# Kernel optimization log

Hardware: AMD Instinct MI355X
Metric: run time of the kernel (lower is better)

## Reference

```python
import jax, jax.numpy as jnp
import numpy as np

N_NODES = 100000
N_EDGES = 1600000
IN_DIM, HID_DIM, OUT_DIM = 128, 64, 64


def _graph_conv(src, dst, h, W, b, n_nodes):
    # DGL GraphConv, norm='both': out = D_in^{-1/2} A (D_out^{-1/2} h W) + b
    ones = jnp.ones(src.shape[0], dtype=h.dtype)
    deg_out = jax.ops.segment_sum(ones, src, num_segments=n_nodes)
    deg_in = jax.ops.segment_sum(ones, dst, num_segments=n_nodes)
    norm_src = jax.lax.rsqrt(jnp.maximum(deg_out, 1.0))  # [N]
    norm_dst = jax.lax.rsqrt(jnp.maximum(deg_in, 1.0))   # [N]
    # project first (in_dim >= out_dim path), then aggregate over edges
    x = (h * norm_src[:, None]) @ W                      # [N, d_out]
    msg = x[src]                                         # [E, d_out] gather
    agg = jax.ops.segment_sum(msg, dst, num_segments=n_nodes)  # [N, d_out]
    return agg * norm_dst[:, None] + b


def setup_inputs() -> dict:
    key = jax.random.key(0)
    k = jax.random.split(key, 6)
    h = jax.random.normal(k[0], (N_NODES, IN_DIM), dtype=jnp.float32)
    src = jax.random.randint(k[1], (N_EDGES,), 0, N_NODES, dtype=jnp.int32)
    dst = jax.random.randint(k[2], (N_EDGES,), 0, N_NODES, dtype=jnp.int32)
    W1 = jax.random.normal(k[3], (IN_DIM, HID_DIM), dtype=jnp.float32) / np.sqrt(IN_DIM)
    b1 = jnp.zeros((HID_DIM,), dtype=jnp.float32)
    W2 = jax.random.normal(k[4], (HID_DIM, OUT_DIM), dtype=jnp.float32) / np.sqrt(HID_DIM)
    b2 = jnp.zeros((OUT_DIM,), dtype=jnp.float32)
    return {"h": h, "src": src, "dst": dst, "W1": W1, "b1": b1, "W2": W2, "b2": b2}


def reference(h, src, dst, W1, b1, W2, b2):
    x = _graph_conv(src, dst, h, W1, b1, N_NODES)
    x = jax.nn.elu(x)  # act = nn.ELU()
    x = _graph_conv(src, dst, x, W2, b2, N_NODES)
    return x  # last_act is None
```

## Files before the change

kernel.cpp:

```cpp
#include <hip/hip_runtime.h>
#include <math.h>

#define CH 4096
#define NBUK_MAX 256
#define MAXB 12288
#define SRC_BITS 17

typedef short bf16x8 __attribute__((ext_vector_type(8)));
typedef float f32x4 __attribute__((ext_vector_type(4)));
typedef float f32x2 __attribute__((ext_vector_type(2)));

__device__ __forceinline__ unsigned short f2bf(float f) {
    union { float f; unsigned int u; } v; v.f = f;
    unsigned int r = (v.u + 0x7FFFu + ((v.u >> 16) & 1u)) >> 16;
    return (unsigned short)r;
}
__device__ __forceinline__ float bf2f(unsigned short u) {
    union { unsigned int u; float f; } v; v.u = ((unsigned int)u) << 16;
    return v.f;
}
__device__ __forceinline__ float bflo(unsigned int u) {
    union { unsigned int u; float f; } v; v.u = u << 16;
    return v.f;
}
__device__ __forceinline__ float bfhi(unsigned int u) {
    union { unsigned int u; float f; } v; v.u = u & 0xFFFF0000u;
    return v.f;
}

__global__ __launch_bounds__(256) void p1a_kernel(const int* __restrict__ src, const int* __restrict__ dst,
                                                  int* __restrict__ mat, int E, int B1, int nbuk) {
    __shared__ int hd[NBUK_MAX], hs[NBUK_MAX];
    const int t = threadIdx.x;
    if (t < nbuk) { hd[t] = 0; hs[t] = 0; }
    __syncthreads();
    const int base = blockIdx.x * CH;
    const int cnt = min(CH, E - base);
    for (int k = t; k < cnt; k += 256) {
        int d = dst[base + k];
        int s = src[base + k];
        atomicAdd(&hd[d >> 9], 1);
        atomicAdd(&hs[s >> 9], 1);
    }
    __syncthreads();
    if (t < nbuk) {
        mat[t * B1 + blockIdx.x] = hd[t];
        mat[(nbuk + t) * B1 + blockIdx.x] = hs[t];
    }
}

__global__ __launch_bounds__(256) void scan1_kernel(const int* __restrict__ cnt,
                                                    int* __restrict__ seg,
                                                    int* __restrict__ bsums, int N) {
    __shared__ int tsum[256];
    const int t = threadIdx.x;
    const int base = blockIdx.x * 1024 + t * 4;
    int v0 = (base + 0 < N) ? cnt[base + 0] : 0;
    int v1 = (base + 1 < N) ? cnt[base + 1] : 0;
    int v2 = (base + 2 < N) ? cnt[base + 2] : 0;
    int v3 = (base + 3 < N) ? cnt[base + 3] : 0;
    tsum[t] = v0 + v1 + v2 + v3;
    __syncthreads();
    for (int off = 1; off < 256; off <<= 1) {
        int x = (t >= off) ? tsum[t - off] : 0;
        __syncthreads();
        if (t >= off) tsum[t] += x;
        __syncthreads();
    }
    int run = (t > 0) ? tsum[t - 1] : 0;
    if (base + 0 < N) seg[base + 0] = run; run += v0;
    if (base + 1 < N) seg[base + 1] = run; run += v1;
    if (base + 2 < N) seg[base + 2] = run; run += v2;
    if (base + 3 < N) seg[base + 3] = run;
    if (t == 255) bsums[blockIdx.x] = tsum[255];
}

__global__ void scan2_kernel(int* __restrict__ bsums, int* __restrict__ seg, int N, int G) {
    __shared__ int s[256];
    int t = threadIdx.x;
    if (t < G) s[t] = bsums[t];
    __syncthreads();
    if (t == 0) {
        int run = 0;
        for (int i = 0; i < G; ++i) { int v = s[i]; s[i] = run; run += v; }
        seg[N] = run;
    }
    __syncthreads();
    if (t < G) bsums[t] = s[t];
}

__global__ __launch_bounds__(256) void scan3_kernel(int* __restrict__ seg,
                                                    const int* __restrict__ bsums, int N) {
    int add = bsums[blockIdx.x];
    int base = blockIdx.x * 1024 + threadIdx.x * 4;
#pragma unroll
    for (int i = 0; i < 4; ++i) {
        int idx = base + i;
        if (idx < N) seg[idx] += add;
    }
}

__global__ __launch_bounds__(256) void p1c_kernel(const int* __restrict__ src, const int* __restrict__ dst,
                                                  const int* __restrict__ mat,
                                                  const int* __restrict__ scan,
                                                  int* __restrict__ pedge,
                                                  int E, int B1, int nbuk) {
    __shared__ int hd[NBUK_MAX], hs[NBUK_MAX];
    __shared__ int curD[NBUK_MAX], curS[NBUK_MAX];
    __shared__ int baseD[NBUK_MAX], baseS[NBUK_MAX];
    __shared__ int stD[CH];
    __shared__ int stS[CH];
    const int t = threadIdx.x;
    if (t < nbuk) {
        hd[t] = mat[t * B1 + blockIdx.x];
        hs[t] = mat[(nbuk + t) * B1 + blockIdx.x];
    }
    const int base = blockIdx.x * CH;
    const int cnt = min(CH, E - base);
    int dl[CH / 256], sl[CH / 256];
#pragma unroll
    for (int k = 0; k < CH / 256; ++k) {
        int i = t + k * 256;
        if (i < cnt) {
            dl[k] = dst[base + i];
            sl[k] = src[base + i];
        }
    }
    __syncthreads();
    for (int off = 1; off < nbuk; off <<= 1) {
        int v0 = (t >= off && t < nbuk) ? hd[t - off] : 0;
        int w0 = (t >= off && t < nbuk) ? hs[t - off] : 0;
        __syncthreads();
        if (t < nbuk) { hd[t] += v0; hs[t] += w0; }
        __syncthreads();
    }
    if (t < nbuk) {
        int excD = t ? hd[t - 1] : 0;
        int excS = t ? hs[t - 1] : 0;
        curD[t] = excD;
        curS[t] = excS;
        baseD[t] = scan[t * B1 + blockIdx.x] - excD;
        baseS[t] = scan[(nbuk + t) * B1 + blockIdx.x] - excS;
    }
    __syncthreads();
#pragma unroll
    for (int k = 0; k < CH / 256; ++k) {
        int i = t + k * 256;
        if (i < cnt) {
            int j = dl[k] >> 9;
            int p = atomicAdd(&curD[j], 1);
            stD[p] = ((dl[k] & 511) << SRC_BITS) | sl[k];
            int jq = sl[k] >> 9;
            int q = atomicAdd(&curS[jq], 1);
            stS[q] = sl[k];
        }
    }
    __syncthreads();
    for (int i = t; i < cnt; i += 256) {
        int lo = 0, hi = nbuk - 1;
        while (lo < hi) { int mid = (lo + hi) >> 1; if (hd[mid] > i) hi = mid; else lo = mid + 1; }
        pedge[baseD[lo] + i] = stD[i];
        int lo2 = 0, hi2 = nbuk - 1;
        while (lo2 < hi2) { int mid = (lo2 + hi2) >> 1; if (hs[mid] > i) hi2 = mid; else lo2 = mid + 1; }
        pedge[baseS[lo2] + i] = stS[i];
    }
}

__global__ __launch_bounds__(512) void p2s2_kernel(const int* __restrict__ pedge,
                                                   const int* __restrict__ scan,
                                                   int* __restrict__ esrc, int* __restrict__ seg,
                                                   float* __restrict__ norm_dst,
                                                   float* __restrict__ norm_src,
                                                   int N, int E, int B1, int nbuk) {
    __shared__ int h[512];
    __shared__ int cur[512];
    __shared__ int stage[MAXB];
    const int t = threadIdx.x;
    const int b0 = blockIdx.x;
    if (b0 >= nbuk) {
        const int b = b0 - nbuk;
        h[t] = 0;
        __syncthreads();
        const int sb0 = scan[(nbuk + b) * B1];
        const int sb1 = scan[(nbuk + b + 1) * B1];
        for (int i = sb0 + t; i < sb1; i += 512) atomicAdd(&h[pedge[i] & 511], 1);
        __syncthreads();
        int n = (b << 9) + t;
        if (n < N) norm_src[n] = rsqrtf(fmaxf((float)h[t], 1.0f));
        return;
    }
    const int b = b0;
    h[t] = 0;
    __syncthreads();
    const int bb0 = scan[b * B1];
    const int bb1 = scan[(b + 1) * B1];
    for (int i = bb0 + t; i < bb1; i += 512) atomicAdd(&h[(pedge[i] >> SRC_BITS) & 511], 1);
    __syncthreads();
    for (int off = 1; off < 512; off <<= 1) {
        int v = (t >= off) ? h[t - off] : 0;
        __syncthreads();
        h[t] += v;
        __syncthreads();
    }
    {
        int exc = t ? h[t - 1] : 0;
        cur[t] = exc;
        int n = (b << 9) + t;
        if (n < N) {
            seg[n] = bb0 + exc;
            norm_dst[n] = rsqrtf(fmaxf((float)(h[t] - exc), 1.0f));
        }
        if (b == 0 && t == 0) seg[N] = E;
    }
    __syncthreads();
    const int cnt = bb1 - bb0;
    for (int i = bb0 + t; i < bb1; i += 512) {
        int v = pedge[i];
        int j = (v >> SRC_BITS) & 511;
        int p = atomicAdd(&cur[j], 1);
        int s = v & ((1 << SRC_BITS) - 1);
        if (p < MAXB) stage[p] = s; else esrc[bb0 + p] = s;
    }
    __syncthreads();
    for (int i = t; i < cnt && i < MAXB; i += 512) esrc[bb0 + i] = stage[i];
}

template<int K>
__global__ __launch_bounds__(256) void gemm_norm(const float* __restrict__ H,
                                                 const float* __restrict__ W,
                                                 const float* __restrict__ norm,
                                                 unsigned short* __restrict__ X, int N) {
    constexpr int KP = K + 8;
    __shared__ __align__(16) unsigned short sHi[64 * KP];
    __shared__ __align__(16) unsigned short sLo[64 * KP];
    const int tid = threadIdx.x;

    for (int idx = tid; idx < K * 64; idx += 256) {
        int k = idx >> 6;
        int c = idx & 63;
        float v = W[idx];
        unsigned short hi = f2bf(v);
        sHi[c * KP + k] = hi;
        sLo[c * KP + k] = f2bf(v - bf2f(hi));
    }
    __syncthreads();

    const int w = tid >> 6;
    const int lane = tid & 63;
    const int quad = lane >> 4;
    const int l16 = lane & 15;
    const int n0 = blockIdx.x * 64;
    const int arow = n0 + w * 16 + l16;
    const int arow_c = (arow < N) ? arow : (N - 1);
    const float* Hrow = H + (size_t)arow_c * K + quad * 8;

    f32x4 acc[4];
#pragma unroll
    for (int t = 0; t < 4; ++t) acc[t] = (f32x4){0.0f, 0.0f, 0.0f, 0.0f};

    float4 p0 = *(const float4*)(Hrow + 0);
    float4 p1 = *(const float4*)(Hrow + 4);

#pragma unroll
    for (int kc = 0; kc < K / 32; ++kc) {
        const float v[8] = {p0.x, p0.y, p0.z, p0.w, p1.x, p1.y, p1.z, p1.w};
        bf16x8 aHi, aLo;
#pragma unroll
        for (int j = 0; j < 8; ++j) {
            unsigned short hi = f2bf(v[j]);
            aHi[j] = (short)hi;
            aLo[j] = (short)f2bf(v[j] - bf2f(hi));
        }
        if (kc + 1 < K / 32) {
            p0 = *(const float4*)(Hrow + (kc + 1) * 32 + 0);
            p1 = *(const float4*)(Hrow + (kc + 1) * 32 + 4);
        }
        const int kbase = kc * 32 + quad * 8;
#pragma unroll
        for (int t = 0; t < 4; ++t) {
            const int col = t * 16 + l16;
            const bf16x8 bHi = *(const bf16x8*)&sHi[col * KP + kbase];
            const bf16x8 bLo = *(const bf16x8*)&sLo[col * KP + kbase];
            acc[t] = __builtin_amdgcn_mfma_f32_16x16x32_bf16(aLo, bHi, acc[t], 0, 0, 0);
            acc[t] = __builtin_amdgcn_mfma_f32_16x16x32_bf16(aHi, bLo, acc[t], 0, 0, 0);
            acc[t] = __builtin_amdgcn_mfma_f32_16x16x32_bf16(aHi, bHi, acc[t], 0, 0, 0);
        }
    }

#pragma unroll
    for (int r = 0; r < 4; ++r) {
        const int node = n0 + w * 16 + quad * 4 + r;
        if (node < N) {
            const float s = norm[node];
#pragma unroll
            for (int t = 0; t < 4; ++t) {
                X[(size_t)node * 64 + t * 16 + l16] = f2bf(acc[t][r] * s);
            }
        } else if (node == N) {
#pragma unroll
            for (int t = 0; t < 4; ++t) {
                X[(size_t)node * 64 + t * 16 + l16] = 0;
            }
        }
    }
}

template<bool ELU>
__global__ __launch_bounds__(256) void segsum_kernel(const unsigned short* __restrict__ X,
                                                     const int* __restrict__ esrc,
                                                     const int* __restrict__ seg,
                                                     const float* __restrict__ norm_dst,
                                                     const float* __restrict__ bias,
                                                     float* __restrict__ out, int N) {
    const int node = __builtin_amdgcn_readfirstlane(blockIdx.x * 4 + (threadIdx.x >> 6));
    if (node >= N) return;
    const int lane = threadIdx.x & 63;
    const int eh = lane >> 3;
    const int fl = lane & 7;
    const unsigned flo = (unsigned)fl << 4;
    const int fown = fl * 8 + ((eh & 1) << 2) + (eh & 2) + (eh >> 2);
    const float bv = bias[fown];
    const int s0 = seg[node];
    const int s1 = seg[node + 1];
    const char* Xb = (const char*)X;
    f32x2 A0 = {0.0f, 0.0f}, A1 = {0.0f, 0.0f}, A2 = {0.0f, 0.0f}, A3 = {0.0f, 0.0f};
#define ACC8(u) \
    A0 += (f32x2){bflo(u.x), bfhi(u.x)}; A1 += (f32x2){bflo(u.y), bfhi(u.y)}; \
    A2 += (f32x2){bflo(u.z), bfhi(u.z)}; A3 += (f32x2){bflo(u.w), bfhi(u.w)};
    int e = s0;
    for (; e + 16 <= s1; e += 16) {
        const int r0 = esrc[e + eh];
        const int r1 = esrc[e + 8 + eh];
        const uint4 u0 = *(const uint4*)(Xb + ((((unsigned)r0) << 7) | flo));
        const uint4 u1 = *(const uint4*)(Xb + ((((unsigned)r1) << 7) | flo));
        ACC8(u0);
        ACC8(u1);
    }
    if (e < s1) {
        const int i0 = e + eh;
        const int i1 = e + 8 + eh;
        const int q0 = esrc[i0];
        const int q1 = esrc[i1];
        const int r0 = (i0 < s1) ? q0 : N;
        const int r1 = (i1 < s1) ? q1 : N;
        const uint4 u0 = *(const uint4*)(Xb + ((((unsigned)r0) << 7) | flo));
        const uint4 u1 = *(const uint4*)(Xb + ((((unsigned)r1) << 7) | flo));
        ACC8(u0);
        ACC8(u1);
    }
#undef ACC8
    float a0 = A0.x, a1 = A0.y, a2 = A1.x, a3 = A1.y;
    float a4 = A2.x, a5 = A2.y, a6 = A3.x, a7 = A3.y;
    const bool p0 = (eh & 1) != 0;
    const bool p1 = (eh & 2) != 0;
    const bool p2 = (eh & 4) != 0;
    float t0, t1, t2, t3;
    {
        float sA = p0 ? a0 : a4, kA = p0 ? a4 : a0;
        float sB = p0 ? a1 : a5, kB = p0 ? a5 : a1;
        float sC = p0 ? a2 : a6, kC = p0 ? a6 : a2;
        float sD = p0 ? a3 : a7, kD = p0 ? a7 : a3;
        t0 = kA + __shfl_xor(sA, 8);
        t1 = kB + __shfl_xor(sB, 8);
        t2 = kC + __shfl_xor(sC, 8);
        t3 = kD + __shfl_xor(sD, 8);
    }
    float u0, u1;
    {
        float sA = p1 ? t0 : t2, kA = p1 ? t2 : t0;
        float sB = p1 ? t1 : t3, kB = p1 ? t3 : t1;
        u0 = kA + __shfl_xor(sA, 16);
        u1 = kB + __shfl_xor(sB, 16);
    }
    float v;
    {
        float sA = p2 ? u0 : u1, kA = p2 ? u1 : u0;
        v = kA + __shfl_xor(sA, 32);
    }
    const float s = norm_dst[node];
    float r = v * s + bv;
    if (ELU) r = r > 0.0f ? r : expm1f(r);
    out[(size_t)node * 64 + fown] = r;
}

extern "C" void kernel_launch(void* const* d_in, const int* in_sizes, int n_in,
                              void* d_out, int out_size, void* d_ws, size_t ws_size,
                              hipStream_t stream) {
    const float* h   = (const float*)d_in[0];
    const int*   src = (const int*)d_in[1];
    const int*   dst = (const int*)d_in[2];
    const float* W1  = (const float*)d_in[3];
    const float* b1  = (const float*)d_in[4];
    const float* W2  = (const float*)d_in[5];
    const float* b2  = (const float*)d_in[6];
    float* out = (float*)d_out;

    const int N = in_sizes[0] / 128;
    const int E = in_sizes[1];
    const int nbuk = (N + 511) >> 9;
    const int B1 = (E + CH - 1) / CH;
    const int M = 2 * nbuk * B1;

    int* iw = (int*)d_ws;
    int* mat   = iw;
    int* scanb = mat + M;
    int* bsums = scanb + M + 4;
    int* pedge = bsums + 256;
    int* esrc  = pedge + 2 * (size_t)E;
    int* seg   = esrc + (size_t)E + 16;
    uintptr_t fp = (uintptr_t)(seg + (size_t)N + 4);
    fp = (fp + 63) & ~(uintptr_t)63;
    float* norm_src = (float*)fp;
    float* norm_dst = norm_src + (size_t)N;
    float* H1       = norm_dst + (size_t)N;
    unsigned short* Xb = (unsigned short*)(H1 + 64 * (size_t)N);

    p1a_kernel<<<B1, 256, 0, stream>>>(src, dst, mat, E, B1, nbuk);
    const int G = (M + 1023) / 1024;
    scan1_kernel<<<G, 256, 0, stream>>>(mat, scanb, bsums, M);
    scan2_kernel<<<1, 256, 0, stream>>>(bsums, scanb, M, G);
    scan3_kernel<<<G, 256, 0, stream>>>(scanb, bsums, M);
    p1c_kernel<<<B1, 256, 0, stream>>>(src, dst, mat, scanb, pedge, E, B1, nbuk);
    p2s2_kernel<<<2 * nbuk, 512, 0, stream>>>(pedge, scanb, esrc, seg, norm_dst, norm_src,
                                              N, E, B1, nbuk);

    const int segGrid = (N + 3) / 4;
    const int gemmGrid = (N + 64) / 64;

    gemm_norm<128><<<gemmGrid, 256, 0, stream>>>(h, W1, norm_src, Xb, N);
    segsum_kernel<true><<<segGrid, 256, 0, stream>>>(Xb, esrc, seg, norm_dst, b1, H1, N);

    gemm_norm<64><<<gemmGrid, 256, 0, stream>>>(H1, W2, norm_src, Xb, N);
    segsum_kernel<false><<<segGrid, 256, 0, stream>>>(Xb, esrc, seg, norm_dst, b2, out, N);
}
```

Measured before the change: 288.1 us.

## Store projected features in 8 feature-chunk planes and split segsum by chunk

The GEMM output X now goes into 8 separate planes of 8 bf16 features (16 bytes per node per plane) instead of 128-byte rows. The segment-sum kernel gives each block one feature chunk, with 8 nodes per wave and 8 lanes per node. Each chunk plane is about 1.6 MB, so the random gathers for one chunk should stay resident in cache. The cost is that the esrc and seg indices are re-read 8 times, one per chunk, and each node's output is written in scattered 32-byte pieces.

```diff
diff --git a/kernel.cpp b/kernel.cpp
--- a/kernel.cpp
+++ b/kernel.cpp
@@ -287,6 +287,8 @@
         }
     }
 
+    const size_t CS = 8 * (size_t)(N + 1);
+    const int sub = l16 & 7;
 #pragma unroll
     for (int r = 0; r < 4; ++r) {
         const int node = n0 + w * 16 + quad * 4 + r;
@@ -294,12 +296,14 @@
             const float s = norm[node];
 #pragma unroll
             for (int t = 0; t < 4; ++t) {
-                X[(size_t)node * 64 + t * 16 + l16] = f2bf(acc[t][r] * s);
+                const int chunk = t * 2 + (l16 >> 3);
+                X[chunk * CS + (size_t)node * 8 + sub] = f2bf(acc[t][r] * s);
             }
         } else if (node == N) {
 #pragma unroll
             for (int t = 0; t < 4; ++t) {
-                X[(size_t)node * 64 + t * 16 + l16] = 0;
+                const int chunk = t * 2 + (l16 >> 3);
+                X[chunk * CS + (size_t)node * 8 + sub] = 0;
             }
         }
     }
@@ -312,75 +316,76 @@
                                                      const float* __restrict__ norm_dst,
                                                      const float* __restrict__ bias,
                                                      float* __restrict__ out, int N) {
-    const int node = __builtin_amdgcn_readfirstlane(blockIdx.x * 4 + (threadIdx.x >> 6));
-    if (node >= N) return;
+    const int c = blockIdx.x & 7;
+    const int g = blockIdx.x >> 3;
     const int lane = threadIdx.x & 63;
-    const int eh = lane >> 3;
-    const int fl = lane & 7;
-    const unsigned flo = (unsigned)fl << 4;
-    const int fown = fl * 8 + ((eh & 1) << 2) + (eh & 2) + (eh >> 2);
-    const float bv = bias[fown];
-    const int s0 = seg[node];
-    const int s1 = seg[node + 1];
-    const char* Xb = (const char*)X;
+    const int slot = lane & 7;
+    const int node = g * 32 + ((threadIdx.x >> 6) << 3) + (lane >> 3);
+    const int frev = ((slot & 1) << 2) | (slot & 2) | (slot >> 2);
+    const char* Xc = (const char*)X + (((size_t)c * (size_t)(N + 1)) << 4);
+    const bool act = node < N;
+    const int s0 = act ? seg[node] : 0;
+    const int s1 = act ? seg[node + 1] : 0;
     f32x2 A0 = {0.0f, 0.0f}, A1 = {0.0f, 0.0f}, A2 = {0.0f, 0.0f}, A3 = {0.0f, 0.0f};
 #define ACC8(u) \
     A0 += (f32x2){bflo(u.x), bfhi(u.x)}; A1 += (f32x2){bflo(u.y), bfhi(u.y)}; \
     A2 += (f32x2){bflo(u.z), bfhi(u.z)}; A3 += (f32x2){bflo(u.w), bfhi(u.w)};
     int e = s0;
     for (; e + 16 <= s1; e += 16) {
-        const int r0 = esrc[e + eh];
-        const int r1 = esrc[e + 8 + eh];
-        const uint4 u0 = *(const uint4*)(Xb + ((((unsigned)r0) << 7) | flo));
-        const uint4 u1 = *(const uint4*)(Xb + ((((unsigned)r1) << 7) | flo));
+        const int r0 = esrc[e + slot];
+        const int r1 = esrc[e + 8 + slot];
+        const uint4 u0 = *(const uint4*)(Xc + (((unsigned)r0) << 4));
+        const uint4 u1 = *(const uint4*)(Xc + (((unsigned)r1) << 4));
         ACC8(u0);
         ACC8(u1);
     }
     if (e < s1) {
-        const int i0 = e + eh;
-        const int i1 = e + 8 + eh;
+        const int i0 = e + slot;
+        const int i1 = e + 8 + slot;
         const int q0 = esrc[i0];
         const int q1 = esrc[i1];
         const int r0 = (i0 < s1) ? q0 : N;
         const int r1 = (i1 < s1) ? q1 : N;
-        const uint4 u0 = *(const uint4*)(Xb + ((((unsigned)r0) << 7) | flo));
-        const uint4 u1 = *(const uint4*)(Xb + ((((unsigned)r1) << 7) | flo));
+        const uint4 u0 = *(const uint4*)(Xc + (((unsigned)r0) << 4));
+        const uint4 u1 = *(const uint4*)(Xc + (((unsigned)r1) << 4));
         ACC8(u0);
         ACC8(u1);
     }
 #undef ACC8
     float a0 = A0.x, a1 = A0.y, a2 = A1.x, a3 = A1.y;
     float a4 = A2.x, a5 = A2.y, a6 = A3.x, a7 = A3.y;
-    const bool p0 = (eh & 1) != 0;
-    const bool p1 = (eh & 2) != 0;
-    const bool p2 = (eh & 4) != 0;
+    const bool q0 = (slot & 1) != 0;
+    const bool q1 = (slot & 2) != 0;
+    const bool q2 = (slot & 4) != 0;
     float t0, t1, t2, t3;
     {
-        float sA = p0 ? a0 : a4, kA = p0 ? a4 : a0;
-        float sB = p0 ? a1 : a5, kB = p0 ? a5 : a1;
-        float sC = p0 ? a2 : a6, kC = p0 ? a6 : a2;
-        float sD = p0 ? a3 : a7, kD = p0 ? a7 : a3;
-        t0 = kA + __shfl_xor(sA, 8);
-        t1 = kB + __shfl_xor(sB, 8);
-        t2 = kC + __shfl_xor(sC, 8);
-        t3 = kD + __shfl_xor(sD, 8);
+        float sA = q0 ? a0 : a4, kA = q0 ? a4 : a0;
+        float sB = q0 ? a1 : a5, kB = q0 ? a5 : a1;
+        float sC = q0 ? a2 : a6, kC = q0 ? a6 : a2;
+        float sD = q0 ? a3 : a7, kD = q0 ? a7 : a3;
+        t0 = kA + __shfl_xor(sA, 1);
+        t1 = kB + __shfl_xor(sB, 1);
+        t2 = kC + __shfl_xor(sC, 1);
+        t3 = kD + __shfl_xor(sD, 1);
     }
     float u0, u1;
     {
-        float sA = p1 ? t0 : t2, kA = p1 ? t2 : t0;
-        float sB = p1 ? t1 : t3, kB = p1 ? t3 : t1;
-        u0 = kA + __shfl_xor(sA, 16);
-        u1 = kB + __shfl_xor(sB, 16);
+        float sA = q1 ? t0 : t2, kA = q1 ? t2 : t0;
+        float sB = q1 ? t1 : t3, kB = q1 ? t3 : t1;
+        u0 = kA + __shfl_xor(sA, 2);
+        u1 = kB + __shfl_xor(sB, 2);
     }
     float v;
     {
-        float sA = p2 ? u0 : u1, kA = p2 ? u1 : u0;
-        v = kA + __shfl_xor(sA, 32);
-    }
-    const float s = norm_dst[node];
-    float r = v * s + bv;
-    if (ELU) r = r > 0.0f ? r : expm1f(r);
-    out[(size_t)node * 64 + fown] = r;
+        float sA = q2 ? u0 : u1, kA = q2 ? u1 : u0;
+        v = kA + __shfl_xor(sA, 4);
+    }
+    if (act) {
+        const float s = norm_dst[node];
+        float r = v * s + bias[c * 8 + frev];
+        if (ELU) r = r > 0.0f ? r : expm1f(r);
+        out[(size_t)node * 64 + c * 8 + frev] = r;
+    }
 }
 
 extern "C" void kernel_launch(void* const* d_in, const int* in_sizes, int n_in,
@@ -424,7 +429,7 @@
     p2s2_kernel<<<2 * nbuk, 512, 0, stream>>>(pedge, scanb, esrc, seg, norm_dst, norm_src,
                                               N, E, B1, nbuk);
 
-    const int segGrid = (N + 3) / 4;
+    const int segGrid = ((N + 31) / 32) * 8;
     const int gemmGrid = (N + 64) / 64;
 
     gemm_norm<128><<<gemmGrid, 256, 0, stream>>>(h, W1, norm_src, Xb, N);
```

Result: slower. 314.4 us (+9.1%).
